# Kernel optimization log

Measured on AMD Instinct MI355X. Metric: run time of the kernel, lower is better.

The kernel has to match this reference:

```python
import jax, jax.numpy as jnp
import numpy as np

B, T, E, L, N, V = 512, 1005, 100, 10, 20, 32000


def prelu(x, a):
    return jnp.where(x >= 0, x, a * x)


def setup_inputs() -> dict:
    key = jax.random.key(0)
    ks = jax.random.split(key, 11)
    s = 0.1  # ~xavier std for 100x100
    return {
        "in_data": jax.random.normal(ks[0], (B, T, E), dtype=jnp.float32),
        "f": jax.random.normal(ks[1], (L, E), dtype=jnp.float32) * s,
        "h0": jax.random.normal(ks[2], (1, N, E), dtype=jnp.float32) * s,
        "w_mem": jax.random.normal(ks[3], (1, N, E), dtype=jnp.float32) * s,
        "U_w": jax.random.normal(ks[4], (E, E), dtype=jnp.float32) * s,
        "V_w": jax.random.normal(ks[5], (E, E), dtype=jnp.float32) * s,
        "W_w": jax.random.normal(ks[6], (E, E), dtype=jnp.float32) * s,
        "a_dm": jnp.full((1,), 0.25, dtype=jnp.float32),
        "H_w": jax.random.normal(ks[7], (E, E), dtype=jnp.float32) * s,
        "H_b": jax.random.normal(ks[8], (E,), dtype=jnp.float32) * s,
        "R_w": jax.random.normal(ks[9], (V, E), dtype=jnp.float32) * s,
        "R_b": jax.random.normal(ks[10], (V,), dtype=jnp.float32) * s,
        "a_out": jnp.full((1,), 0.25, dtype=jnp.float32),
    }


def reference(in_data, f, h0, w_mem, U_w, V_w, W_w, a_dm, H_w, H_b, R_w, R_b, a_out):
    n_full = T // L  # rest = T % L != 0 by construction -> torch loop runs n_full times
    rest = T % L
    # InputEncoder over all full sentences at once: [B, n_full, E]
    chunks = in_data[:, : n_full * L].reshape(B, n_full, L, E)
    infos = jnp.einsum("le,bnle->bne", f, chunks)
    # precompute V(w) term (constant across steps): [1, N, E]
    Vw = jnp.einsum("one,fe->onf", w_mem, V_w)

    def step(h, s):  # h: [B,N,E], s: [B,E]
        g = jax.nn.sigmoid(jnp.einsum("bne,be->bn", h + w_mem, s))[..., None]
        cand = prelu(
            jnp.einsum("bne,fe->bnf", h, U_w)
            + Vw
            + jnp.einsum("be,fe->bf", s, W_w)[:, None, :],
            a_dm,
        )
        h = h + g * cand
        h = h / jnp.linalg.norm(h, axis=2, keepdims=True)
        return h, None

    h_init = jnp.broadcast_to(h0, (B, N, E))
    h, _ = jax.lax.scan(step, h_init, jnp.swapaxes(infos, 0, 1))  # scan over sentences

    # query = InputEncoder on trailing remainder tokens
    q_tok = in_data[:, n_full * L :]  # [B, rest, E]
    q = jnp.einsum("le,ble->be", f[:rest], q_tok)  # [B, E]

    # OutputModule
    p = jax.nn.softmax(jnp.einsum("bne,be->bn", h, q), axis=1)  # [B, N]
    u = jnp.einsum("bn,bne->be", p, h)  # [B, E]
    y = q + u @ H_w.T + H_b
    return prelu(y, a_out) @ R_w.T + R_b  # [B, V]
```

## Files before the change

kernel.cpp:

```cpp
#include <hip/hip_runtime.h>
#include <hip/hip_bf16.h>

#define E      100
#define E2     112
#define NSLOT  20
#define BB     512
#define TT     1005
#define NFULL  100
#define LL     10
#define REST   5
#define VV     32000

typedef _Float16 f16x8 __attribute__((ext_vector_type(8)));
typedef _Float16 f16x4 __attribute__((ext_vector_type(4)));
typedef float    f32x16 __attribute__((ext_vector_type(16)));

__global__ __launch_bounds__(256) void k_cvt(
    const float* __restrict__ R_w, const float* __restrict__ W_w,
    const float* __restrict__ w_mem,
    _Float16* __restrict__ R16, _Float16* __restrict__ Wm16)
{
    const int gid = blockIdx.x * 256 + threadIdx.x;
    {
        int v = gid / 28, e4 = gid % 28;
        f16x4 o;
        if (e4 < 25) {
            float4 x = *(const float4*)&R_w[(size_t)v * E + e4 * 4];
            o[0] = (_Float16)x.x; o[1] = (_Float16)x.y;
            o[2] = (_Float16)x.z; o[3] = (_Float16)x.w;
        } else { o[0] = o[1] = o[2] = o[3] = (_Float16)0.f; }
        *(f16x4*)&R16[(size_t)v * E2 + e4 * 4] = o;
    }
    if (gid < 128 * 28) {
        int j = gid / 28, e4 = gid % 28;
        f16x4 o; o[0] = o[1] = o[2] = o[3] = (_Float16)0.f;
        if (e4 < 25 && j < 120) {
            float4 x = (j < 100) ? *(const float4*)&W_w[j * E + e4 * 4]
                                 : *(const float4*)&w_mem[(j - 100) * E + e4 * 4];
            o[0] = (_Float16)x.x; o[1] = (_Float16)x.y;
            o[2] = (_Float16)x.z; o[3] = (_Float16)x.w;
        }
        *(f16x4*)&Wm16[j * E2 + e4 * 4] = o;
    }
}

__global__ __launch_bounds__(256, 2) void k_prep(
    const float* __restrict__ in_data, const float* __restrict__ f,
    _Float16* __restrict__ s16, float* __restrict__ q_all)
{
    __shared__ float4 f4s[250];
    const int tid = threadIdx.x;
    const int b   = blockIdx.x;
    if (tid < 250) f4s[tid] = ((const float4*)f)[tid];
    __syncthreads();

    const size_t base = (size_t)b * TT * E;
    for (int idx = tid; idx < 2500; idx += 256) {
        int n = idx / 25, e4 = idx - n * 25;
        float4 a; a.x = a.y = a.z = a.w = 0.f;
        const float* xp = in_data + base + (size_t)(n * LL) * E + e4 * 4;
        #pragma unroll
        for (int l = 0; l < LL; ++l) {
            float4 x = *(const float4*)(xp + l * E);
            float4 fv = f4s[l * 25 + e4];
            a.x += fv.x * x.x; a.y += fv.y * x.y;
            a.z += fv.z * x.z; a.w += fv.w * x.w;
        }
        f16x4 o;
        o[0] = (_Float16)a.x; o[1] = (_Float16)a.y;
        o[2] = (_Float16)a.z; o[3] = (_Float16)a.w;
        *(f16x4*)&s16[((size_t)n * BB + b) * E2 + e4 * 4] = o;
    }
    for (int idx = tid; idx < 600; idx += 256) {
        int n = idx / 6, k = idx - n * 6;
        ((unsigned int*)s16)[(((size_t)n * BB + b) * E2 + 100) / 2 + k] = 0u;
    }
    if (tid < E) {
        const float* fp = (const float*)f4s;
        float a = 0.f;
        #pragma unroll
        for (int l = 0; l < REST; ++l)
            a += fp[l * E + tid] * in_data[base + (size_t)(NFULL * LL + l) * E + tid];
        q_all[(size_t)b * E + tid] = a;
    }
}

__global__ __launch_bounds__(256, 2) void k_mm(
    const _Float16* __restrict__ s16, const _Float16* __restrict__ Wm16,
    _Float16* __restrict__ sws16)
{
    __shared__ __align__(16) _Float16 AF[14 * 128 * 8];
    __shared__ __align__(16) _Float16 BF[14 * 128 * 8];
    const int tid  = threadIdx.x;
    const int mb   = blockIdx.x;
    const int lane = tid & 63;
    const int wv   = tid >> 6;
    const int half = lane >> 5;
    const int jt   = wv * 32 + (lane & 31);

    for (int idx = tid; idx < 128 * 14; idx += 256) {
        int m = idx / 14, c8 = idx - m * 14;
        *(f16x8*)&AF[(c8 * 128 + m) * 8] =
            *(const f16x8*)&s16[((size_t)mb * 128 + m) * E2 + c8 * 8];
        *(f16x8*)&BF[(c8 * 128 + m) * 8] =
            *(const f16x8*)&Wm16[m * E2 + c8 * 8];
    }
    __syncthreads();

    f16x8 Bfr[7];
    #pragma unroll
    for (int ck = 0; ck < 7; ++ck)
        Bfr[ck] = *(const f16x8*)&BF[((ck * 2 + half) * 128 + jt) * 8];

    #pragma unroll
    for (int Mt = 0; Mt < 4; ++Mt) {
        f32x16 acc;
        #pragma unroll
        for (int r = 0; r < 16; ++r) acc[r] = 0.f;
        #pragma unroll
        for (int ck = 0; ck < 7; ++ck) {
            f16x8 a = *(const f16x8*)&AF[((ck * 2 + half) * 128 + 32 * Mt + (lane & 31)) * 8];
            acc = __builtin_amdgcn_mfma_f32_32x32x16_f16(a, Bfr[ck], acc, 0, 0, 0);
        }
        #pragma unroll
        for (int r = 0; r < 16; ++r) {
            int row = 32 * Mt + (r & 3) + 8 * (r >> 2) + 4 * half;
            sws16[((size_t)mb * 128 + row) * 128 + jt] = (_Float16)acc[r];
        }
    }
}

#define BAR() do { asm volatile("s_waitcnt lgkmcnt(0)" ::: "memory"); \
                   __builtin_amdgcn_s_barrier(); } while (0)

__global__ __launch_bounds__(256, 2) void k_scan(
    const float* __restrict__ h0, const float* __restrict__ w_mem,
    const float* __restrict__ U_w, const float* __restrict__ V_w,
    const float* __restrict__ a_dm,
    const _Float16* __restrict__ s16, const _Float16* __restrict__ sws16,
    float* __restrict__ h_final)
{
    __shared__ __align__(16) _Float16 h16f[2][7 * 64 * 8];

    const int tid  = threadIdx.x;
    const int b    = blockIdx.x;
    const int lane = tid & 63;
    const int wv   = tid >> 6;
    const int col  = lane & 31;
    const int half = lane >> 5;
    const float adm = a_dm[0];
    const int cg   = (col < NSLOT) ? col : 0;

    int wb[4];
    #pragma unroll
    for (int q = 0; q < 4; ++q) {
        int bp = (4 * wv + q) * 512 + col * 16 + 8 * half;
        wb[q] = bp ^ (((bp >> 9) & 3) << 5);
    }
    int rb[7];
    #pragma unroll
    for (int ck = 0; ck < 7; ++ck) {
        int bp = ck * 1024 + lane * 16;
        rb[ck] = bp ^ (((bp >> 9) & 3) << 5);
    }

    f16x8 Uf[7];
    const int fA = 32 * wv + col;
    #pragma unroll
    for (int ck = 0; ck < 7; ++ck) {
        #pragma unroll
        for (int j = 0; j < 8; ++j) {
            int e = 16 * ck + 8 * half + j;
            Uf[ck][j] = (_Float16)((fA < E && e < E) ? U_w[fA * E + e] : 0.f);
        }
    }
    float VwC[16], hC[16];
    #pragma unroll
    for (int r = 0; r < 16; ++r) { VwC[r] = 0.f; hC[r] = 0.f; }
    for (int e4 = 0; e4 < 25; ++e4) {
        float4 w4 = make_float4(0.f, 0.f, 0.f, 0.f);
        if (col < NSLOT) w4 = *(const float4*)&w_mem[col * E + e4 * 4];
        #pragma unroll
        for (int r = 0; r < 16; ++r) {
            int f = 32 * wv + (r & 3) + 8 * (r >> 2) + 4 * half;
            if (f < E) {
                float4 v4 = *(const float4*)&V_w[f * E + e4 * 4];
                VwC[r] += w4.x * v4.x + w4.y * v4.y + w4.z * v4.z + w4.w * v4.w;
            }
        }
    }
    #pragma unroll
    for (int r = 0; r < 16; ++r) {
        int f = 32 * wv + (r & 3) + 8 * (r >> 2) + 4 * half;
        if (col < NSLOT && f < E) hC[r] = h0[col * E + f];
    }
    for (int idx = tid; idx < 1792; idx += 256)
        ((float2*)h16f)[idx] = make_float2(0.f, 0.f);
    __syncthreads();
    if (col < NSLOT) {
        #pragma unroll
        for (int q = 0; q < 4; ++q) {
            int f0 = 32 * wv + 4 * half + 8 * q;
            if (f0 < E) {
                f16x4 pk;
                #pragma unroll
                for (int i = 0; i < 4; ++i) pk[i] = (_Float16)hC[4 * q + i];
                *(f16x4*)((char*)h16f[0] + wb[q]) = pk;
            }
        }
    } else if (col == NSLOT) {
        #pragma unroll
        for (int q = 0; q < 4; ++q) {
            int f0 = 32 * wv + 4 * half + 8 * q;
            if (f0 < E)
                *(f16x4*)((char*)h16f[0] + wb[q]) =
                    *(const f16x4*)&s16[(size_t)b * E2 + f0];
        }
    }
    f16x4 cur_sw[4];
    _Float16 cur_swn;
    {
        const size_t r0 = (size_t)b * 128;
        #pragma unroll
        for (int q = 0; q < 4; ++q) {
            int f0 = 32 * wv + 4 * half + 8 * q;
            if (f0 < E) cur_sw[q] = *(const f16x4*)&sws16[r0 + f0];
            else { cur_sw[q][0] = cur_sw[q][1] = cur_sw[q][2] = cur_sw[q][3] = (_Float16)0.f; }
        }
        cur_swn = sws16[r0 + 100 + cg];
    }
    __syncthreads();

    for (int t = 0; t < NFULL; ++t) {
        const int p = t & 1;

        const int tn = (t + 1 < NFULL) ? (t + 1) : t;
        const size_t rown = (size_t)tn * BB + b;
        f16x4 nxt_sw[4], nxt_s[4];
        _Float16 nxt_swn;
        #pragma unroll
        for (int q = 0; q < 4; ++q) {
            int f0 = 32 * wv + 4 * half + 8 * q;
            if (f0 < E) nxt_sw[q] = *(const f16x4*)&sws16[rown * 128 + f0];
            else { nxt_sw[q][0] = nxt_sw[q][1] = nxt_sw[q][2] = nxt_sw[q][3] = (_Float16)0.f; }
        }
        nxt_swn = sws16[rown * 128 + 100 + cg];
        if (col == NSLOT) {
            #pragma unroll
            for (int q = 0; q < 4; ++q) {
                int f0 = 32 * wv + 4 * half + 8 * q;
                if (f0 < E) nxt_s[q] = *(const f16x4*)&s16[rown * E2 + f0];
            }
        }

        const char* hb = (const char*)h16f[p];
        f16x8 hB[7];
        #pragma unroll
        for (int ck = 0; ck < 7; ++ck)
            hB[ck] = *(const f16x8*)(hb + rb[ck]);

        f32x16 acc, acc2;
        #pragma unroll
        for (int r = 0; r < 16; ++r) { acc[r] = 0.f; acc2[r] = 0.f; }
        #pragma unroll
        for (int ck = 0; ck < 7; ++ck) {
            acc  = __builtin_amdgcn_mfma_f32_32x32x16_f16(Uf[ck], hB[ck], acc,  0, 0, 0);
            acc2 = __builtin_amdgcn_mfma_f32_32x32x16_f16(hB[ck], hB[ck], acc2, 0, 0, 0);
        }

        float nv = 0.f;
        #pragma unroll
        for (int r = 0; r < 16; ++r) {
            const int row = (r & 3) + 8 * (r >> 2) + 4 * half;
            if (row == col) nv = acc2[r];
        }
        float gv = half ? acc2[8] : 0.f;
        nv += __shfl_xor(nv, 32);
        gv += __shfl_xor(gv, 32);

        float rn = (t == 0) ? 1.f : __builtin_amdgcn_rsqf(nv);
        float dd = fmaf(rn, gv, (float)cur_swn);
        float g  = __builtin_amdgcn_rcpf(1.f + __expf(-dd));

        char* hw = (char*)h16f[p ^ 1];
        if (col < NSLOT) {
            #pragma unroll
            for (int q = 0; q < 4; ++q) {
                int f0 = 32 * wv + 4 * half + 8 * q;
                if (f0 < E) {
                    f16x4 pk;
                    #pragma unroll
                    for (int i = 0; i < 4; ++i) {
                        int r = 4 * q + i;
                        float c = fmaf(rn, acc[r], VwC[r] + (float)cur_sw[q][i]);
                        c = (c >= 0.f) ? c : adm * c;
                        float hnew = fmaf(rn, hC[r], g * c);
                        hC[r] = hnew;
                        pk[i] = (_Float16)hnew;
                    }
                    *(f16x4*)(hw + wb[q]) = pk;
                }
            }
        } else if (col == NSLOT) {
            #pragma unroll
            for (int q = 0; q < 4; ++q) {
                int f0 = 32 * wv + 4 * half + 8 * q;
                if (f0 < E) *(f16x4*)(hw + wb[q]) = nxt_s[q];
            }
        }
        #pragma unroll
        for (int q = 0; q < 4; ++q) cur_sw[q] = nxt_sw[q];
        cur_swn = nxt_swn;

        BAR();
    }

    {
        const char* hb = (const char*)h16f[0];
        f16x8 hB[7];
        #pragma unroll
        for (int ck = 0; ck < 7; ++ck)
            hB[ck] = *(const f16x8*)(hb + rb[ck]);
        f32x16 acc2;
        #pragma unroll
        for (int r = 0; r < 16; ++r) acc2[r] = 0.f;
        #pragma unroll
        for (int ck = 0; ck < 7; ++ck)
            acc2 = __builtin_amdgcn_mfma_f32_32x32x16_f16(hB[ck], hB[ck], acc2, 0, 0, 0);
        float nv = 0.f;
        #pragma unroll
        for (int r = 0; r < 16; ++r) {
            const int row = (r & 3) + 8 * (r >> 2) + 4 * half;
            if (row == col) nv = acc2[r];
        }
        nv += __shfl_xor(nv, 32);
        float rn = __builtin_amdgcn_rsqf(nv);
        if (col < NSLOT) {
            #pragma unroll
            for (int q = 0; q < 4; ++q) {
                int f0 = 32 * wv + 4 * half + 8 * q;
                if (f0 < E) {
                    float4 o;
                    o.x = rn * hC[4 * q + 0];
                    o.y = rn * hC[4 * q + 1];
                    o.z = rn * hC[4 * q + 2];
                    o.w = rn * hC[4 * q + 3];
                    *(float4*)&h_final[(size_t)b * NSLOT * E + col * E + f0] = o;
                }
            }
        }
    }
}

__global__ __launch_bounds__(256, 2) void k_attn(
    const float* __restrict__ h_final, const float* __restrict__ q_all,
    const float* __restrict__ H_w, const float* __restrict__ H_b,
    const float* __restrict__ a_out, _Float16* __restrict__ py16)
{
    __shared__ float Hl[E * 101];
    __shared__ float h_l[NSLOT * E];
    __shared__ float q_l[E], u_l[E];
    __shared__ float part[200], party[200];
    __shared__ float dl[NSLOT], pl[NSLOT];
    const int tid = threadIdx.x;
    const int b   = blockIdx.x;

    for (int idx = tid; idx < E * E; idx += 256) {
        int fr = idx / E, e = idx - fr * E;
        Hl[fr * 101 + e] = H_w[idx];
    }
    for (int idx = tid; idx < NSLOT * E; idx += 256)
        h_l[idx] = h_final[(size_t)b * NSLOT * E + idx];
    if (tid < E) q_l[tid] = q_all[(size_t)b * E + tid];
    __syncthreads();

    if (tid < 200) {
        int n = tid / 10, j = tid - n * 10;
        float a = 0.f;
        #pragma unroll
        for (int k = 0; k < 10; ++k) { int e = j * 10 + k; a += h_l[n * E + e] * q_l[e]; }
        part[tid] = a;
    }
    __syncthreads();
    if (tid < NSLOT) {
        float d = 0.f;
        #pragma unroll
        for (int j = 0; j < 10; ++j) d += part[tid * 10 + j];
        dl[tid] = d;
    }
    __syncthreads();
    if (tid < NSLOT) {
        float m = -1e30f;
        for (int i = 0; i < NSLOT; ++i) m = fmaxf(m, dl[i]);
        float s = 0.f;
        for (int i = 0; i < NSLOT; ++i) s += __expf(dl[i] - m);
        pl[tid] = __expf(dl[tid] - m) / s;
    }
    __syncthreads();
    if (tid < E) {
        float u = 0.f;
        for (int n = 0; n < NSLOT; ++n) u += pl[n] * h_l[n * E + tid];
        u_l[tid] = u;
    }
    __syncthreads();
    if (tid < 200) {
        int fr = tid % E, hf = tid / E;
        float a = 0.f;
        for (int e = hf * 50; e < hf * 50 + 50; ++e) a += u_l[e] * Hl[fr * 101 + e];
        party[tid] = a;
    }
    __syncthreads();
    if (tid < E2) {
        if (tid < E) {
            float y = q_l[tid] + H_b[tid] + party[tid] + party[100 + tid];
            const float ao = a_out[0];
            y = (y >= 0.f) ? y : ao * y;
            py16[(size_t)b * E2 + tid] = (_Float16)y;
        } else py16[(size_t)b * E2 + tid] = (_Float16)0.f;
    }
}

__global__ __launch_bounds__(256, 2) void k_out(
    const _Float16* __restrict__ py16, const _Float16* __restrict__ R16,
    const float* __restrict__ R_b, float* __restrict__ out)
{
    __shared__ __align__(16) _Float16 AF[14 * 128 * 8];
    __shared__ __align__(16) _Float16 BF[14 * 128 * 8];
    const int tid  = threadIdx.x;
    const int vb   = blockIdx.x;
    const int mb   = blockIdx.y;
    const int lane = tid & 63;
    const int wv   = tid >> 6;
    const int half = lane >> 5;
    const int jt   = wv * 32 + (lane & 31);
    const int v0   = vb * 128;

    for (int idx = tid; idx < 128 * 14; idx += 256) {
        int m = idx / 14, c8 = idx - m * 14;
        *(f16x8*)&AF[(c8 * 128 + m) * 8] =
            *(const f16x8*)&py16[((size_t)mb * 128 + m) * E2 + c8 * 8];
        *(f16x8*)&BF[(c8 * 128 + m) * 8] =
            *(const f16x8*)&R16[(size_t)(v0 + m) * E2 + c8 * 8];
    }
    __syncthreads();

    f16x8 Bfr[7];
    #pragma unroll
    for (int ck = 0; ck < 7; ++ck)
        Bfr[ck] = *(const f16x8*)&BF[((ck * 2 + half) * 128 + jt) * 8];
    const float rbv = R_b[v0 + jt];

    #pragma unroll
    for (int Mt = 0; Mt < 4; ++Mt) {
        f32x16 acc;
        #pragma unroll
        for (int r = 0; r < 16; ++r) acc[r] = 0.f;
        #pragma unroll
        for (int ck = 0; ck < 7; ++ck) {
            f16x8 a = *(const f16x8*)&AF[((ck * 2 + half) * 128 + 32 * Mt + (lane & 31)) * 8];
            acc = __builtin_amdgcn_mfma_f32_32x32x16_f16(a, Bfr[ck], acc, 0, 0, 0);
        }
        #pragma unroll
        for (int r = 0; r < 16; ++r) {
            int row = 32 * Mt + (r & 3) + 8 * (r >> 2) + 4 * half;
            out[((size_t)mb * 128 + row) * VV + v0 + jt] = acc[r] + rbv;
        }
    }
}

extern "C" void kernel_launch(void* const* d_in, const int* in_sizes, int n_in,
                              void* d_out, int out_size, void* d_ws, size_t ws_size,
                              hipStream_t stream)
{
    const float* in_data = (const float*)d_in[0];
    const float* f       = (const float*)d_in[1];
    const float* h0      = (const float*)d_in[2];
    const float* w_mem   = (const float*)d_in[3];
    const float* U_w     = (const float*)d_in[4];
    const float* V_w     = (const float*)d_in[5];
    const float* W_w     = (const float*)d_in[6];
    const float* a_dm    = (const float*)d_in[7];
    const float* H_w     = (const float*)d_in[8];
    const float* H_b     = (const float*)d_in[9];
    const float* R_w     = (const float*)d_in[10];
    const float* R_b     = (const float*)d_in[11];
    const float* a_out   = (const float*)d_in[12];
    float* out = (float*)d_out;

    char* ws = (char*)d_ws;
    _Float16* s16    = (_Float16*)(ws);
    _Float16* sws16  = (_Float16*)(ws + 11468800);
    _Float16* R16    = (_Float16*)(ws + 24576000);
    _Float16* Wm16   = (_Float16*)(ws + 31744000);
    float*    q_all  = (float*)   (ws + 31772672);
    float*    h_fin  = (float*)   (ws + 31977472);
    _Float16* py16   = (_Float16*)(ws + 36073472);

    k_cvt <<<3500, 256, 0, stream>>>(R_w, W_w, w_mem, R16, Wm16);
    k_prep<<<BB, 256, 0, stream>>>(in_data, f, s16, q_all);
    k_mm  <<<400, 256, 0, stream>>>(s16, Wm16, sws16);
    k_scan<<<BB, 256, 0, stream>>>(h0, w_mem, U_w, V_w, a_dm, s16, sws16, h_fin);
    k_attn<<<BB, 256, 0, stream>>>(h_fin, q_all, H_w, H_b, a_out, py16);
    k_out <<<dim3(VV / 128, 4), 256, 0, stream>>>(py16, R16, R_b, out);
}
```

Baseline: 581.9 us.

## Fold norm/gate into U matmul, fuse R_w conversion blocks into scan launch

The scan step drops the separate h·h Gram MFMA. Wave 3 instead swaps the unused padding rows of its U fragment for h rows, so the same MFMA also yields the row norms and gate dot products. Those scalars are broadcast through shared memory, which costs an extra barrier per step. The final norm is computed from the fp32 register values with an LDS reduction. The large R_w fp16 conversion now runs as extra trailing blocks of the scan kernel, so it can overlap the latency-bound scan, while the W_w conversion stays a tiny separate kernel.

Result: slower. 665.6 us (+14.4%).

```diff
diff --git a/kernel.cpp b/kernel.cpp
--- a/kernel.cpp
+++ b/kernel.cpp
@@ -15,13 +15,124 @@
 typedef _Float16 f16x4 __attribute__((ext_vector_type(4)));
 typedef float    f32x16 __attribute__((ext_vector_type(16)));
 
-__global__ __launch_bounds__(256) void k_cvt(
-    const float* __restrict__ R_w, const float* __restrict__ W_w,
-    const float* __restrict__ w_mem,
-    _Float16* __restrict__ R16, _Float16* __restrict__ Wm16)
+__global__ __launch_bounds__(256) void k_cvtw(
+    const float* __restrict__ W_w, const float* __restrict__ w_mem,
+    _Float16* __restrict__ Wm16)
 {
     const int gid = blockIdx.x * 256 + threadIdx.x;
-    {
+    int j = gid / 28, e4 = gid % 28;
+    f16x4 o; o[0] = o[1] = o[2] = o[3] = (_Float16)0.f;
+    if (e4 < 25 && j < 120) {
+        float4 x = (j < 100) ? *(const float4*)&W_w[j * E + e4 * 4]
+                             : *(const float4*)&w_mem[(j - 100) * E + e4 * 4];
+        o[0] = (_Float16)x.x; o[1] = (_Float16)x.y;
+        o[2] = (_Float16)x.z; o[3] = (_Float16)x.w;
+    }
+    *(f16x4*)&Wm16[j * E2 + e4 * 4] = o;
+}
+
+__global__ __launch_bounds__(256, 2) void k_prep(
+    const float* __restrict__ in_data, const float* __restrict__ f,
+    _Float16* __restrict__ s16, float* __restrict__ q_all)
+{
+    __shared__ float4 f4s[250];
+    const int tid = threadIdx.x;
+    const int b   = blockIdx.x;
+    if (tid < 250) f4s[tid] = ((const float4*)f)[tid];
+    __syncthreads();
+
+    const size_t base = (size_t)b * TT * E;
+    for (int idx = tid; idx < 2500; idx += 256) {
+        int n = idx / 25, e4 = idx - n * 25;
+        float4 a; a.x = a.y = a.z = a.w = 0.f;
+        const float* xp = in_data + base + (size_t)(n * LL) * E + e4 * 4;
+        #pragma unroll
+        for (int l = 0; l < LL; ++l) {
+            float4 x = *(const float4*)(xp + l * E);
+            float4 fv = f4s[l * 25 + e4];
+            a.x += fv.x * x.x; a.y += fv.y * x.y;
+            a.z += fv.z * x.z; a.w += fv.w * x.w;
+        }
+        f16x4 o;
+        o[0] = (_Float16)a.x; o[1] = (_Float16)a.y;
+        o[2] = (_Float16)a.z; o[3] = (_Float16)a.w;
+        *(f16x4*)&s16[((size_t)n * BB + b) * E2 + e4 * 4] = o;
+    }
+    for (int idx = tid; idx < 600; idx += 256) {
+        int n = idx / 6, k = idx - n * 6;
+        ((unsigned int*)s16)[(((size_t)n * BB + b) * E2 + 100) / 2 + k] = 0u;
+    }
+    if (tid < E) {
+        const float* fp = (const float*)f4s;
+        float a = 0.f;
+        #pragma unroll
+        for (int l = 0; l < REST; ++l)
+            a += fp[l * E + tid] * in_data[base + (size_t)(NFULL * LL + l) * E + tid];
+        q_all[(size_t)b * E + tid] = a;
+    }
+}
+
+__global__ __launch_bounds__(256, 2) void k_mm(
+    const _Float16* __restrict__ s16, const _Float16* __restrict__ Wm16,
+    _Float16* __restrict__ sws16)
+{
+    __shared__ __align__(16) _Float16 AF[14 * 128 * 8];
+    __shared__ __align__(16) _Float16 BF[14 * 128 * 8];
+    const int tid  = threadIdx.x;
+    const int mb   = blockIdx.x;
+    const int lane = tid & 63;
+    const int wv   = tid >> 6;
+    const int half = lane >> 5;
+    const int jt   = wv * 32 + (lane & 31);
+
+    for (int idx = tid; idx < 128 * 14; idx += 256) {
+        int m = idx / 14, c8 = idx - m * 14;
+        *(f16x8*)&AF[(c8 * 128 + m) * 8] =
+            *(const f16x8*)&s16[((size_t)mb * 128 + m) * E2 + c8 * 8];
+        *(f16x8*)&BF[(c8 * 128 + m) * 8] =
+            *(const f16x8*)&Wm16[m * E2 + c8 * 8];
+    }
+    __syncthreads();
+
+    f16x8 Bfr[7];
+    #pragma unroll
+    for (int ck = 0; ck < 7; ++ck)
+        Bfr[ck] = *(const f16x8*)&BF[((ck * 2 + half) * 128 + jt) * 8];
+
+    #pragma unroll
+    for (int Mt = 0; Mt < 4; ++Mt) {
+        f32x16 acc;
+        #pragma unroll
+        for (int r = 0; r < 16; ++r) acc[r] = 0.f;
+        #pragma unroll
+        for (int ck = 0; ck < 7; ++ck) {
+            f16x8 a = *(const f16x8*)&AF[((ck * 2 + half) * 128 + 32 * Mt + (lane & 31)) * 8];
+            acc = __builtin_amdgcn_mfma_f32_32x32x16_f16(a, Bfr[ck], acc, 0, 0, 0);
+        }
+        #pragma unroll
+        for (int r = 0; r < 16; ++r) {
+            int row = 32 * Mt + (r & 3) + 8 * (r >> 2) + 4 * half;
+            sws16[((size_t)mb * 128 + row) * 128 + jt] = (_Float16)acc[r];
+        }
+    }
+}
+
+#define BAR() do { asm volatile("s_waitcnt lgkmcnt(0)" ::: "memory"); \
+                   __builtin_amdgcn_s_barrier(); } while (0)
+
+__global__ __launch_bounds__(256, 2) void k_scan(
+    const float* __restrict__ h0, const float* __restrict__ w_mem,
+    const float* __restrict__ U_w, const float* __restrict__ V_w,
+    const float* __restrict__ a_dm,
+    const _Float16* __restrict__ s16, const _Float16* __restrict__ sws16,
+    float* __restrict__ h_final,
+    const float* __restrict__ R_w, _Float16* __restrict__ R16)
+{
+    const int tid = threadIdx.x;
+    const int bid = blockIdx.x;
+
+    if (bid >= BB) {
+        const int gid = (bid - BB) * 256 + tid;
         int v = gid / 28, e4 = gid % 28;
         f16x4 o;
         if (e4 < 25) {
@@ -30,120 +141,14 @@
             o[2] = (_Float16)x.z; o[3] = (_Float16)x.w;
         } else { o[0] = o[1] = o[2] = o[3] = (_Float16)0.f; }
         *(f16x4*)&R16[(size_t)v * E2 + e4 * 4] = o;
-    }
-    if (gid < 128 * 28) {
-        int j = gid / 28, e4 = gid % 28;
-        f16x4 o; o[0] = o[1] = o[2] = o[3] = (_Float16)0.f;
-        if (e4 < 25 && j < 120) {
-            float4 x = (j < 100) ? *(const float4*)&W_w[j * E + e4 * 4]
-                                 : *(const float4*)&w_mem[(j - 100) * E + e4 * 4];
-            o[0] = (_Float16)x.x; o[1] = (_Float16)x.y;
-            o[2] = (_Float16)x.z; o[3] = (_Float16)x.w;
-        }
-        *(f16x4*)&Wm16[j * E2 + e4 * 4] = o;
-    }
-}
-
-__global__ __launch_bounds__(256, 2) void k_prep(
-    const float* __restrict__ in_data, const float* __restrict__ f,
-    _Float16* __restrict__ s16, float* __restrict__ q_all)
-{
-    __shared__ float4 f4s[250];
-    const int tid = threadIdx.x;
-    const int b   = blockIdx.x;
-    if (tid < 250) f4s[tid] = ((const float4*)f)[tid];
-    __syncthreads();
-
-    const size_t base = (size_t)b * TT * E;
-    for (int idx = tid; idx < 2500; idx += 256) {
-        int n = idx / 25, e4 = idx - n * 25;
-        float4 a; a.x = a.y = a.z = a.w = 0.f;
-        const float* xp = in_data + base + (size_t)(n * LL) * E + e4 * 4;
-        #pragma unroll
-        for (int l = 0; l < LL; ++l) {
-            float4 x = *(const float4*)(xp + l * E);
-            float4 fv = f4s[l * 25 + e4];
-            a.x += fv.x * x.x; a.y += fv.y * x.y;
-            a.z += fv.z * x.z; a.w += fv.w * x.w;
-        }
-        f16x4 o;
-        o[0] = (_Float16)a.x; o[1] = (_Float16)a.y;
-        o[2] = (_Float16)a.z; o[3] = (_Float16)a.w;
-        *(f16x4*)&s16[((size_t)n * BB + b) * E2 + e4 * 4] = o;
-    }
-    for (int idx = tid; idx < 600; idx += 256) {
-        int n = idx / 6, k = idx - n * 6;
-        ((unsigned int*)s16)[(((size_t)n * BB + b) * E2 + 100) / 2 + k] = 0u;
-    }
-    if (tid < E) {
-        const float* fp = (const float*)f4s;
-        float a = 0.f;
-        #pragma unroll
-        for (int l = 0; l < REST; ++l)
-            a += fp[l * E + tid] * in_data[base + (size_t)(NFULL * LL + l) * E + tid];
-        q_all[(size_t)b * E + tid] = a;
-    }
-}
-
-__global__ __launch_bounds__(256, 2) void k_mm(
-    const _Float16* __restrict__ s16, const _Float16* __restrict__ Wm16,
-    _Float16* __restrict__ sws16)
-{
-    __shared__ __align__(16) _Float16 AF[14 * 128 * 8];
-    __shared__ __align__(16) _Float16 BF[14 * 128 * 8];
-    const int tid  = threadIdx.x;
-    const int mb   = blockIdx.x;
-    const int lane = tid & 63;
-    const int wv   = tid >> 6;
-    const int half = lane >> 5;
-    const int jt   = wv * 32 + (lane & 31);
-
-    for (int idx = tid; idx < 128 * 14; idx += 256) {
-        int m = idx / 14, c8 = idx - m * 14;
-        *(f16x8*)&AF[(c8 * 128 + m) * 8] =
-            *(const f16x8*)&s16[((size_t)mb * 128 + m) * E2 + c8 * 8];
-        *(f16x8*)&BF[(c8 * 128 + m) * 8] =
-            *(const f16x8*)&Wm16[m * E2 + c8 * 8];
-    }
-    __syncthreads();
-
-    f16x8 Bfr[7];
-    #pragma unroll
-    for (int ck = 0; ck < 7; ++ck)
-        Bfr[ck] = *(const f16x8*)&BF[((ck * 2 + half) * 128 + jt) * 8];
-
-    #pragma unroll
-    for (int Mt = 0; Mt < 4; ++Mt) {
-        f32x16 acc;
-        #pragma unroll
-        for (int r = 0; r < 16; ++r) acc[r] = 0.f;
-        #pragma unroll
-        for (int ck = 0; ck < 7; ++ck) {
-            f16x8 a = *(const f16x8*)&AF[((ck * 2 + half) * 128 + 32 * Mt + (lane & 31)) * 8];
-            acc = __builtin_amdgcn_mfma_f32_32x32x16_f16(a, Bfr[ck], acc, 0, 0, 0);
-        }
-        #pragma unroll
-        for (int r = 0; r < 16; ++r) {
-            int row = 32 * Mt + (r & 3) + 8 * (r >> 2) + 4 * half;
-            sws16[((size_t)mb * 128 + row) * 128 + jt] = (_Float16)acc[r];
-        }
-    }
-}
-
-#define BAR() do { asm volatile("s_waitcnt lgkmcnt(0)" ::: "memory"); \
-                   __builtin_amdgcn_s_barrier(); } while (0)
-
-__global__ __launch_bounds__(256, 2) void k_scan(
-    const float* __restrict__ h0, const float* __restrict__ w_mem,
-    const float* __restrict__ U_w, const float* __restrict__ V_w,
-    const float* __restrict__ a_dm,
-    const _Float16* __restrict__ s16, const _Float16* __restrict__ sws16,
-    float* __restrict__ h_final)
-{
+        return;
+    }
+
     __shared__ __align__(16) _Float16 h16f[2][7 * 64 * 8];
-
-    const int tid  = threadIdx.x;
-    const int b    = blockIdx.x;
+    __shared__ __align__(16) float2   nggL[32];
+    __shared__ __align__(16) float    finL[NSLOT * 8];
+
+    const int b    = bid;
     const int lane = tid & 63;
     const int wv   = tid >> 6;
     const int col  = lane & 31;
@@ -157,12 +162,15 @@
         int bp = (4 * wv + q) * 512 + col * 16 + 8 * half;
         wb[q] = bp ^ (((bp >> 9) & 3) << 5);
     }
-    int rb[7];
+    int rb[7], rA[7];
     #pragma unroll
     for (int ck = 0; ck < 7; ++ck) {
         int bp = ck * 1024 + lane * 16;
         rb[ck] = bp ^ (((bp >> 9) & 3) << 5);
-    }
+        int ba = ck * 1024 + (lane - 4) * 16;
+        rA[ck] = ba ^ (((ba >> 9) & 3) << 5);
+    }
+    const bool a_act = (wv == 3) && (col >= 4) && (col <= 24);
 
     f16x8 Uf[7];
     const int fA = 32 * wv + col;
@@ -254,34 +262,39 @@
         }
 
         const char* hb = (const char*)h16f[p];
+        #pragma unroll
+        for (int ck = 0; ck < 7; ++ck)
+            if (a_act) Uf[ck] = *(const f16x8*)(hb + rA[ck]);
         f16x8 hB[7];
         #pragma unroll
         for (int ck = 0; ck < 7; ++ck)
             hB[ck] = *(const f16x8*)(hb + rb[ck]);
 
-        f32x16 acc, acc2;
-        #pragma unroll
-        for (int r = 0; r < 16; ++r) { acc[r] = 0.f; acc2[r] = 0.f; }
-        #pragma unroll
-        for (int ck = 0; ck < 7; ++ck) {
-            acc  = __builtin_amdgcn_mfma_f32_32x32x16_f16(Uf[ck], hB[ck], acc,  0, 0, 0);
-            acc2 = __builtin_amdgcn_mfma_f32_32x32x16_f16(hB[ck], hB[ck], acc2, 0, 0, 0);
-        }
-
-        float nv = 0.f;
-        #pragma unroll
-        for (int r = 0; r < 16; ++r) {
-            const int row = (r & 3) + 8 * (r >> 2) + 4 * half;
-            if (row == col) nv = acc2[r];
-        }
-        float gv = half ? acc2[8] : 0.f;
-        nv += __shfl_xor(nv, 32);
-        gv += __shfl_xor(gv, 32);
-
-        float rn = (t == 0) ? 1.f : __builtin_amdgcn_rsqf(nv);
-        float dd = fmaf(rn, gv, (float)cur_swn);
-        float g  = __builtin_amdgcn_rcpf(1.f + __expf(-dd));
-
+        f32x16 acc;
+        #pragma unroll
+        for (int r = 0; r < 16; ++r) acc[r] = 0.f;
+        #pragma unroll
+        for (int ck = 0; ck < 7; ++ck)
+            acc = __builtin_amdgcn_mfma_f32_32x32x16_f16(Uf[ck], hB[ck], acc, 0, 0, 0);
+
+        if (wv == 3) {
+            float nv = 0.f;
+            #pragma unroll
+            for (int r = 0; r < 16; ++r) {
+                const int pat = (r & 3) + 8 * (r >> 2) + 4 * half;
+                if (pat == col + 4) nv = acc[r];
+            }
+            nv += __shfl_xor(nv, 32);
+            float gr = half ? 0.f : acc[12];
+            gr += __shfl_xor(gr, 32);
+            float rn = (t == 0) ? 1.f : __builtin_amdgcn_rsqf(nv);
+            float dd = fmaf(rn, gr, (float)cur_swn);
+            float g  = __builtin_amdgcn_rcpf(1.f + __expf(-dd));
+            if (half == 0 && col < NSLOT) nggL[col] = make_float2(rn, g);
+        }
+        BAR();
+
+        const float2 rg = nggL[cg];
         char* hw = (char*)h16f[p ^ 1];
         if (col < NSLOT) {
             #pragma unroll
@@ -292,9 +305,9 @@
                     #pragma unroll
                     for (int i = 0; i < 4; ++i) {
                         int r = 4 * q + i;
-                        float c = fmaf(rn, acc[r], VwC[r] + (float)cur_sw[q][i]);
+                        float c = fmaf(rg.x, acc[r], VwC[r] + (float)cur_sw[q][i]);
                         c = (c >= 0.f) ? c : adm * c;
-                        float hnew = fmaf(rn, hC[r], g * c);
+                        float hnew = fmaf(rg.x, hC[r], rg.y * c);
                         hC[r] = hnew;
                         pk[i] = (_Float16)hnew;
                     }
@@ -316,24 +329,17 @@
     }
 
     {
-        const char* hb = (const char*)h16f[0];
-        f16x8 hB[7];
-        #pragma unroll
-        for (int ck = 0; ck < 7; ++ck)
-            hB[ck] = *(const f16x8*)(hb + rb[ck]);
-        f32x16 acc2;
-        #pragma unroll
-        for (int r = 0; r < 16; ++r) acc2[r] = 0.f;
-        #pragma unroll
-        for (int ck = 0; ck < 7; ++ck)
-            acc2 = __builtin_amdgcn_mfma_f32_32x32x16_f16(hB[ck], hB[ck], acc2, 0, 0, 0);
+        float np = 0.f;
+        #pragma unroll
+        for (int r = 0; r < 16; ++r) np = fmaf(hC[r], hC[r], np);
+        if (col < NSLOT) finL[col * 8 + wv * 2 + half] = np;
+        BAR();
         float nv = 0.f;
-        #pragma unroll
-        for (int r = 0; r < 16; ++r) {
-            const int row = (r & 3) + 8 * (r >> 2) + 4 * half;
-            if (row == col) nv = acc2[r];
-        }
-        nv += __shfl_xor(nv, 32);
+        if (col < NSLOT) {
+            const float4* fp = (const float4*)&finL[col * 8];
+            float4 x = fp[0], y = fp[1];
+            nv = x.x + x.y + x.z + x.w + y.x + y.y + y.z + y.w;
+        }
         float rn = __builtin_amdgcn_rsqf(nv);
         if (col < NSLOT) {
             #pragma unroll
@@ -496,10 +502,11 @@
     float*    h_fin  = (float*)   (ws + 31977472);
     _Float16* py16   = (_Float16*)(ws + 36073472);
 
-    k_cvt <<<3500, 256, 0, stream>>>(R_w, W_w, w_mem, R16, Wm16);
+    k_cvtw<<<14, 256, 0, stream>>>(W_w, w_mem, Wm16);
     k_prep<<<BB, 256, 0, stream>>>(in_data, f, s16, q_all);
     k_mm  <<<400, 256, 0, stream>>>(s16, Wm16, sws16);
-    k_scan<<<BB, 256, 0, stream>>>(h0, w_mem, U_w, V_w, a_dm, s16, sws16, h_fin);
+    k_scan<<<BB + 3500, 256, 0, stream>>>(h0, w_mem, U_w, V_w, a_dm, s16, sws16,
+                                          h_fin, R_w, R16);
     k_attn<<<BB, 256, 0, stream>>>(h_fin, q_all, H_w, H_b, a_out, py16);
     k_out <<<dim3(VV / 128, 4), 256, 0, stream>>>(py16, R16, R_b, out);
 }
```
